# Optimization experiments

Measured on AMD Instinct MI355X. Metric: run time of the kernel, lower is better.

The kernel has to match this reference:

```python
import jax, jax.numpy as jnp
import numpy as np

B, H = 16384, 64          # batch, human_num
SELF_DIM, HUMAN_DIM = 6, 7
D = 32                    # gcn2_w1_dim / embedding dim


def _lin(key, fin, fout):
    return jax.random.normal(key, (fin, fout), jnp.float32) / np.sqrt(fin)


def setup_inputs() -> dict:
    key = jax.random.key(0)
    ks = jax.random.split(key, 40)
    inp = {}
    inp["state"] = jax.random.normal(ks[0], (B, H, SELF_DIM + HUMAN_DIM), jnp.float32)
    inp["dropout"] = 0
    # w_r: mlp(6 -> 64 -> 32, last_relu=True)
    inp["wr_w1"] = _lin(ks[1], SELF_DIM, 64); inp["wr_b1"] = jnp.zeros(64, jnp.float32)
    inp["wr_w2"] = _lin(ks[2], 64, D);        inp["wr_b2"] = jnp.zeros(D, jnp.float32)
    # w_h: mlp(7 -> 64 -> 32, last_relu=True)
    inp["wh_w1"] = _lin(ks[3], HUMAN_DIM, 64); inp["wh_b1"] = jnp.zeros(64, jnp.float32)
    inp["wh_w2"] = _lin(ks[4], 64, D);         inp["wh_b2"] = jnp.zeros(D, jnp.float32)
    # hetero GraphConv weights: per edge type (rh: robot->human, hr: human->robot, hh: human->human),
    # per layer. GraphConv: out = lin_rel(scatter_sum(x_src)) + lin_root(x_dst); lin_root has no bias.
    i = 5
    for L in (1, 2):
        for et in ("rh", "hr", "hh"):
            inp[f"rel_{et}{L}"] = _lin(ks[i], D, D); i += 1
            inp[f"brel_{et}{L}"] = jnp.zeros(D, jnp.float32)
            inp[f"root_{et}{L}"] = _lin(ks[i], D, D); i += 1
    # value_net: mlp(32 -> 150 -> 100 -> 1), no last relu
    inp["vn_w1"] = _lin(ks[i], D, 150);  inp["vn_b1"] = jnp.zeros(150, jnp.float32); i += 1
    inp["vn_w2"] = _lin(ks[i], 150, 100); inp["vn_b2"] = jnp.zeros(100, jnp.float32); i += 1
    inp["vn_w3"] = _lin(ks[i], 100, 1);  inp["vn_b3"] = jnp.zeros(1, jnp.float32)
    return inp


def _hetero_layer(r, h, rel_rh, brel_rh, root_rh, rel_hr, brel_hr, root_hr,
                  rel_hh, brel_hh, root_hh):
    # r: [B, D] robot nodes; h: [B, H, D] human nodes
    sum_h = h.sum(axis=1)  # [B, D]
    # robot receives scatter-sum over all humans (star graph, one robot target)
    new_r = jax.nn.relu(sum_h @ rel_hr + brel_hr + r @ root_hr)
    # each human receives: robot message + sum of all OTHER humans (full graph minus self-loops)
    agg_hh = sum_h[:, None, :] - h  # [B, H, D]
    new_h = jax.nn.relu((r @ rel_rh)[:, None, :] + brel_rh
                        + agg_hh @ rel_hh + brel_hh
                        + h @ root_rh + h @ root_hh)
    return new_r, new_h


def _forward(state, wr_w1, wr_b1, wr_w2, wr_b2, wh_w1, wh_b1, wh_w2, wh_b2,
             rel_rh1, brel_rh1, root_rh1, rel_hr1, brel_hr1, root_hr1,
             rel_hh1, brel_hh1, root_hh1,
             rel_rh2, brel_rh2, root_rh2, rel_hr2, brel_hr2, root_hr2,
             rel_hh2, brel_hh2, root_hh2,
             vn_w1, vn_b1, vn_w2, vn_b2, vn_w3, vn_b3):
    self_state = state[:, 0, :SELF_DIM]        # [B, 6]
    human_states = state[:, :, SELF_DIM:]      # [B, H, 7]
    r = jax.nn.relu(jax.nn.relu(self_state @ wr_w1 + wr_b1) @ wr_w2 + wr_b2)      # [B, D]
    h = jax.nn.relu(jax.nn.relu(human_states @ wh_w1 + wh_b1) @ wh_w2 + wh_b2)    # [B, H, D]
    r, h = _hetero_layer(r, h, rel_rh1, brel_rh1, root_rh1, rel_hr1, brel_hr1,
                         root_hr1, rel_hh1, brel_hh1, root_hh1)
    r, h = _hetero_layer(r, h, rel_rh2, brel_rh2, root_rh2, rel_hr2, brel_hr2,
                         root_hr2, rel_hh2, brel_hh2, root_hh2)
    v = jax.nn.relu(r @ vn_w1 + vn_b1)
    v = jax.nn.relu(v @ vn_w2 + vn_b2)
    return v @ vn_w3 + vn_b3                    # [B, 1]


def reference(state, dropout, wr_w1, wr_b1, wr_w2, wr_b2, wh_w1, wh_b1, wh_w2, wh_b2,
              rel_rh1, brel_rh1, root_rh1, rel_hr1, brel_hr1, root_hr1,
              rel_hh1, brel_hh1, root_hh1,
              rel_rh2, brel_rh2, root_rh2, rel_hr2, brel_hr2, root_hr2,
              rel_hh2, brel_hh2, root_hh2,
              vn_w1, vn_b1, vn_w2, vn_b2, vn_w3, vn_b3):
    # dropout is accepted but unused (matches the torch forward signature)
    return _forward(state, wr_w1, wr_b1, wr_w2, wr_b2, wh_w1, wh_b1, wh_w2, wh_b2,
                    rel_rh1, brel_rh1, root_rh1, rel_hr1, brel_hr1, root_hr1,
                    rel_hh1, brel_hh1, root_hh1,
                    rel_rh2, brel_rh2, root_rh2, rel_hr2, brel_hr2, root_hr2,
                    rel_hh2, brel_hh2, root_hh2,
                    vn_w1, vn_b1, vn_w2, vn_b2, vn_w3, vn_b3)
```

## Files before the change

kernel.cpp:

```cpp
#include <hip/hip_runtime.h>

#define BTOT 16384

typedef __attribute__((ext_vector_type(8))) short bf16x8;
typedef __attribute__((ext_vector_type(4))) float f32x4;

#define MFMA16(a,b,c) __builtin_amdgcn_mfma_f32_16x16x32_bf16((a),(b),(c),0,0,0)

#if __has_builtin(__builtin_amdgcn_cvt_pk_bf16_f32)
typedef __attribute__((ext_vector_type(2))) __bf16 hwbf2;
static __device__ __forceinline__ unsigned pk2(float a, float b) {
    hwbf2 v = __builtin_amdgcn_cvt_pk_bf16_f32(a, b);
    return __builtin_bit_cast(unsigned, v);
}
#else
static __device__ __forceinline__ unsigned pk2(float a, float b) {
    unsigned ua = __float_as_uint(a), ub = __float_as_uint(b);
    unsigned ra = (ua + 0x7FFFu + ((ua >> 16) & 1u)) >> 16;
    unsigned rb = (ub + 0x7FFFu + ((ub >> 16) & 1u)) >> 16;
    return (ra & 0xFFFFu) | (rb << 16);
}
#endif
static __device__ __forceinline__ unsigned short bfhi(float x) {
    return (unsigned short)(pk2(x, 0.f) & 0xFFFFu);
}
static __device__ __forceinline__ float b2f(unsigned short h) {
    return __uint_as_float(((unsigned)h) << 16);
}
static __device__ __forceinline__ short f2s(float x) { return (short)bfhi(x); }
static __device__ __forceinline__ unsigned short bfhi_m(float x) {
    unsigned u = __float_as_uint(x);
    return (unsigned short)((u + 0x7FFFu + ((u >> 16) & 1u)) >> 16);
}
static __device__ __forceinline__ unsigned short bflo_m(float x) {
    unsigned short h = bfhi_m(x);
    return bfhi_m(x - b2f(h));
}
static __device__ __forceinline__ bf16x8 zero8() {
    bf16x8 v;
    #pragma unroll
    for (int i = 0; i < 8; ++i) v[i] = 0;
    return v;
}

__global__ void pack_frags(
    const float* __restrict__ wh_w1, const float* __restrict__ wh_b1,
    const float* __restrict__ wh_w2,
    const float* __restrict__ root_rh1, const float* __restrict__ root_hh1,
    const float* __restrict__ rel_hh1,
    const float* __restrict__ wr_w2,
    const float* __restrict__ rel_hr1, const float* __restrict__ root_hr1,
    const float* __restrict__ rel_rh1,
    const float* __restrict__ rel_hr2, const float* __restrict__ root_hr2,
    const float* __restrict__ vn_w1, const float* __restrict__ vn_w2,
    const float* __restrict__ brel_hr1, const float* __restrict__ brel_rh1,
    const float* __restrict__ brel_hh1, const float* __restrict__ brel_hr2,
    short* __restrict__ pk)
{
    int t = blockIdx.x * blockDim.x + threadIdx.x;
    if (t < 52736) {
        int f = t >> 9, r = t & 511;
        int lane = r >> 3, j = r & 7;
        int q = lane >> 4, c = lane & 15;
        int k = q * 8 + j;
        unsigned short outv;
        if (f < 4) {
            int m = f * 16 + c;
            float v = (k < 7) ? wh_w1[k * 64 + m] : (k == 7 ? wh_b1[m] : 0.f);
            outv = bfhi_m(v);
        } else if (f < 8) {
            int u = f - 4, ks = u >> 1, nt = u & 1;
            int kr = ks * 32 + (j >> 2) * 16 + q * 4 + (j & 3);
            outv = bfhi_m(wh_w2[kr * 32 + nt * 16 + c]);
        } else if (f < 10) {
            int n = (f - 8) * 16 + c;
            int ko = (k >> 1) + ((k & 1) << 4);
            outv = bfhi_m(root_rh1[ko * 32 + n] + root_hh1[ko * 32 + n] - rel_hh1[ko * 32 + n]);
        } else if (f < 22) {
            int u = f - 10, ks = u >> 1, nt = u & 1;
            int kp = ks * 32 + k;
            float w = wr_w2[(kp & 63) * 32 + nt * 16 + c];
            outv = (kp < 128) ? bfhi_m(w) : bflo_m(w);
        } else if (f < 46) {
            int u = f - 22, ks = u >> 2, nt = u & 3;
            int kp = ks * 32 + k, seg = kp >> 5, kk = kp & 31;
            int n2 = (nt & 1) * 16 + c;
            bool sPart = (seg < 2) || (seg == 4);
            const float* W = (nt < 2) ? (sPart ? rel_hr1 : root_hr1)
                                      : (sPart ? rel_hh1 : rel_rh1);
            float w = W[kk * 32 + n2];
            outv = (seg < 4) ? bfhi_m(w) : bflo_m(w);
        } else if (f < 58) {
            int u = f - 46, ks = u >> 1, nt = u & 1;
            int kp = ks * 32 + k, seg = kp >> 5, kk = kp & 31;
            int n = nt * 16 + c;
            bool sPart = (seg < 2) || (seg == 4);
            const float* W = sPart ? rel_hr2 : root_hr2;
            float w = W[kk * 32 + n];
            outv = (seg < 4) ? bfhi_m(w) : bflo_m(w);
        } else if (f < 68) {
            int n = (f - 58) * 16 + c;
            outv = (n < 150) ? bfhi_m(vn_w1[k * 150 + n]) : 0;
        } else {
            int u = f - 68, kt = u / 7, nt = u - kt * 7;
            int kk = kt * 32 + k, n = nt * 16 + c;
            outv = (kk < 150 && n < 100) ? bfhi_m(vn_w2[kk * 100 + n]) : 0;
        }
        pk[t] = (short)outv;
    } else if (t < 52800) {
        int i = t - 52736;
        float* bp = (float*)(pk + 52736);
        bp[i] = (i < 32) ? brel_hr1[i] : brel_rh1[i - 32] + brel_hh1[i - 32];
    } else if (t < 52832) {
        int i = t - 52800;
        float* bp = (float*)(pk + 52864);
        bp[i] = brel_hr2[i];
    }
}

__global__ __launch_bounds__(256) void fused_main(
    const float* __restrict__ state, const short* __restrict__ pk,
    const float* __restrict__ wr_w1, const float* __restrict__ wr_b1,
    const float* __restrict__ wr_b2, const float* __restrict__ wh_b2,
    short* __restrict__ r2buf)
{
    __shared__ __align__(16) short wbuf[4][4096];

    const int tid = threadIdx.x;
    const int wv = tid >> 6, lane = tid & 63;
    const int q = lane >> 4, c = lane & 15;
    const int b = blockIdx.x * 4 + wv;
    const float* st = state + (size_t)b * 832;
    short* T = wbuf[wv];

    const bf16x8* pk16 = (const bf16x8*)pk;
    const float* bg1f = (const float*)(pk + 52736);
    const float* bg2f = (const float*)(pk + 52864);
    const f32x4 z4 = {0.f, 0.f, 0.f, 0.f};

    bf16x8 A1[4], Bh2v[4], Bev[2];
    #pragma unroll
    for (int i = 0; i < 4; ++i) A1[i] = pk16[i * 64 + lane];
    #pragma unroll
    for (int i = 0; i < 4; ++i) Bh2v[i] = pk16[(4 + i) * 64 + lane];
    #pragma unroll
    for (int i = 0; i < 2; ++i) Bev[i] = pk16[(8 + i) * 64 + lane];

    {
        float hf[7];
        #pragma unroll
        for (int m = 0; m < 7; ++m) hf[m] = st[lane * 13 + 6 + m];
        uint4 v = make_uint4(pk2(hf[0], hf[1]), pk2(hf[2], hf[3]),
                             pk2(hf[4], hf[5]), pk2(hf[6], 1.0f));
        *(uint4*)(T + lane * 8) = v;
    }

    float trh;
    {
        float acc = wr_b1[lane];
        #pragma unroll
        for (int m = 0; m < 6; ++m) acc = fmaf(st[m], wr_w1[m * 64 + lane], acc);
        trh = fmaxf(acc, 0.f);
    }

    asm volatile("s_waitcnt lgkmcnt(0)" ::: "memory");

    bf16x8 bx[4];
    #pragma unroll
    for (int ht = 0; ht < 4; ++ht) {
        bf16x8 v = zero8();
        if (q == 0) v = *(const bf16x8*)(T + (ht * 16 + c) * 8);
        bx[ht] = v;
    }

    #pragma unroll
    for (int mhp = 0; mhp < 2; ++mhp) {
        #pragma unroll
        for (int ht = 0; ht < 4; ++ht) {
            f32x4 d0 = MFMA16(A1[2 * mhp + 0], bx[ht], z4);
            f32x4 d1 = MFMA16(A1[2 * mhp + 1], bx[ht], z4);
            d0 = __builtin_elementwise_max(d0, z4);
            d1 = __builtin_elementwise_max(d1, z4);
            uint4 w = make_uint4(pk2(d0[0], d0[1]), pk2(d0[2], d0[3]),
                                 pk2(d1[0], d1[1]), pk2(d1[2], d1[3]));
            int row = ht * 16 + c;
            int p = (mhp * 4 + q) ^ (c & 7);
            *(uint4*)(T + row * 64 + p * 8) = w;
        }
    }

    asm volatile("s_waitcnt lgkmcnt(0)" ::: "memory");

    const float b2a = wh_b2[c], b2b = wh_b2[16 + c];
    const f32x4 b2a4 = {b2a, b2a, b2a, b2a}, b2b4 = {b2b, b2b, b2b, b2b};
    f32x4 psv0 = z4, psv1 = z4;
    #pragma unroll
    for (int mt = 0; mt < 4; ++mt) {
        int row = mt * 16 + c;
        bf16x8 a0 = *(const bf16x8*)(T + row * 64 + ((q ^ (c & 7))) * 8);
        bf16x8 a1 = *(const bf16x8*)(T + row * 64 + (((q + 4) ^ (c & 7))) * 8);
        f32x4 e0 = MFMA16(a0, Bh2v[0], z4); e0 = MFMA16(a1, Bh2v[2], e0);
        f32x4 e1 = MFMA16(a0, Bh2v[1], z4); e1 = MFMA16(a1, Bh2v[3], e1);
        e0 = __builtin_elementwise_max(e0 + b2a4, z4);
        e1 = __builtin_elementwise_max(e1 + b2b4, z4);
        psv0 += e0; psv1 += e1;
        #pragma unroll
        for (int r = 0; r < 4; ++r) {
            int hrow = mt * 16 + q * 4 + r;
            *(unsigned*)(T + hrow * 32 + (((c >> 2) ^ r)) * 8 + (c & 3) * 2) = pk2(e0[r], e1[r]);
        }
    }
    float ps0 = (psv0[0] + psv0[1]) + (psv0[2] + psv0[3]);
    float ps1 = (psv1[0] + psv1[1]) + (psv1[2] + psv1[3]);
    ps0 += __shfl_xor(ps0, 16); ps0 += __shfl_xor(ps0, 32);
    ps1 += __shfl_xor(ps1, 16); ps1 += __shfl_xor(ps1, 32);

    {
        short* SB = T + 3712;
        if (q == 0) {
            unsigned short h0 = bfhi(ps0), h1 = bfhi(ps1);
            SB[c] = (short)h0;        SB[16 + c] = (short)h1;
            SB[32 + c] = (short)bfhi(ps0 - b2f(h0));
            SB[48 + c] = (short)bfhi(ps1 - b2f(h1));
        }
        short* TR = T + 3840;
        unsigned short th = bfhi(trh);
        TR[lane] = (short)th;
        TR[64 + lane] = (short)bfhi(trh - b2f(th));
    }
    __syncthreads();

    const short* rowS = wbuf[c & 3];

    bf16x8 at0 = *(const bf16x8*)(rowS + 3840 + q * 8);
    bf16x8 at1 = *(const bf16x8*)(rowS + 3872 + q * 8);
    bf16x8 at2 = *(const bf16x8*)(rowS + 3904 + q * 8);
    bf16x8 at3 = *(const bf16x8*)(rowS + 3936 + q * 8);
    f32x4 dr0 = z4, dr1 = z4;
    dr0 = MFMA16(at0, pk16[10 * 64 + lane], dr0); dr1 = MFMA16(at0, pk16[11 * 64 + lane], dr1);
    dr0 = MFMA16(at1, pk16[12 * 64 + lane], dr0); dr1 = MFMA16(at1, pk16[13 * 64 + lane], dr1);
    dr0 = MFMA16(at2, pk16[14 * 64 + lane], dr0); dr1 = MFMA16(at2, pk16[15 * 64 + lane], dr1);
    dr0 = MFMA16(at3, pk16[16 * 64 + lane], dr0); dr1 = MFMA16(at3, pk16[17 * 64 + lane], dr1);
    dr0 = MFMA16(at0, pk16[18 * 64 + lane], dr0); dr1 = MFMA16(at0, pk16[19 * 64 + lane], dr1);
    dr0 = MFMA16(at1, pk16[20 * 64 + lane], dr0); dr1 = MFMA16(at1, pk16[21 * 64 + lane], dr1);

    {
        const float wb0 = wr_b2[c], wb1 = wr_b2[16 + c];
        if (q == 0) {
            #pragma unroll
            for (int r = 0; r < 4; ++r) {
                float v0 = fmaxf(dr0[r] + wb0, 0.f), v1 = fmaxf(dr1[r] + wb1, 0.f);
                unsigned short h0 = bfhi(v0), h1 = bfhi(v1);
                T[2048 + r * 32 + c]      = (short)h0;
                T[2048 + r * 32 + 16 + c] = (short)h1;
                T[2176 + r * 32 + c]      = (short)bfhi(v0 - b2f(h0));
                T[2176 + r * 32 + 16 + c] = (short)bfhi(v1 - b2f(h1));
            }
        }
    }
    asm volatile("s_waitcnt lgkmcnt(0)" ::: "memory");

    bf16x8 as0 = *(const bf16x8*)(rowS + 3712 + q * 8);
    bf16x8 as1 = *(const bf16x8*)(rowS + 3744 + q * 8);
    bf16x8 ar0 = *(const bf16x8*)(T + 2048 + (c & 3) * 32 + q * 8);
    bf16x8 ar1 = *(const bf16x8*)(T + 2176 + (c & 3) * 32 + q * 8);
    f32x4 dg[4] = {z4, z4, z4, z4};
    #pragma unroll
    for (int nt = 0; nt < 4; ++nt) dg[nt] = MFMA16(as0, pk16[(22 +  0 + nt) * 64 + lane], dg[nt]);
    #pragma unroll
    for (int nt = 0; nt < 4; ++nt) dg[nt] = MFMA16(as1, pk16[(22 +  4 + nt) * 64 + lane], dg[nt]);
    #pragma unroll
    for (int nt = 0; nt < 4; ++nt) dg[nt] = MFMA16(ar0, pk16[(22 +  8 + nt) * 64 + lane], dg[nt]);
    #pragma unroll
    for (int nt = 0; nt < 4; ++nt) dg[nt] = MFMA16(ar1, pk16[(22 + 12 + nt) * 64 + lane], dg[nt]);
    #pragma unroll
    for (int nt = 0; nt < 4; ++nt) dg[nt] = MFMA16(as0, pk16[(22 + 16 + nt) * 64 + lane], dg[nt]);
    #pragma unroll
    for (int nt = 0; nt < 4; ++nt) dg[nt] = MFMA16(ar0, pk16[(22 + 20 + nt) * 64 + lane], dg[nt]);

    const float c10 = __shfl(dg[2][wv], c) + bg1f[32 + c];
    const float c11 = __shfl(dg[3][wv], c) + bg1f[48 + c];

    {
        if (q == 0) {
            const float gb0 = bg1f[c], gb1 = bg1f[16 + c];
            #pragma unroll
            for (int r = 0; r < 4; ++r) {
                float v0 = fmaxf(dg[0][r] + gb0, 0.f), v1 = fmaxf(dg[1][r] + gb1, 0.f);
                unsigned short h0 = bfhi(v0), h1 = bfhi(v1);
                T[2304 + r * 32 + c]      = (short)h0;
                T[2304 + r * 32 + 16 + c] = (short)h1;
                T[2432 + r * 32 + c]      = (short)bfhi(v0 - b2f(h0));
                T[2432 + r * 32 + 16 + c] = (short)bfhi(v1 - b2f(h1));
            }
        }
    }

    {
        const f32x4 c10v = {c10, c10, c10, c10}, c11v = {c11, c11, c11, c11};
        f32x4 acc0 = z4, acc1 = z4;
        #pragma unroll
        for (int mt = 0; mt < 4; ++mt) {
            int row = mt * 16 + c;
            bf16x8 ah = *(const bf16x8*)(T + row * 32 + ((q ^ (c & 3))) * 8);
            f32x4 g0 = MFMA16(ah, Bev[0], z4);
            f32x4 g1 = MFMA16(ah, Bev[1], z4);
            acc0 += __builtin_elementwise_max(g0 + c10v, z4);
            acc1 += __builtin_elementwise_max(g1 + c11v, z4);
        }
        float t0 = (acc0[0] + acc0[1]) + (acc0[2] + acc0[3]);
        float t1 = (acc1[0] + acc1[1]) + (acc1[2] + acc1[3]);
        t0 += __shfl_xor(t0, 16); t0 += __shfl_xor(t0, 32);
        t1 += __shfl_xor(t1, 16); t1 += __shfl_xor(t1, 32);
        short* G2 = T + 3520;
        if (q == 0) {
            unsigned short h0 = bfhi(t0), h1 = bfhi(t1);
            G2[c] = (short)h0;        G2[16 + c] = (short)h1;
            G2[32 + c] = (short)bfhi(t0 - b2f(h0));
            G2[48 + c] = (short)bfhi(t1 - b2f(h1));
        }
    }
    __syncthreads();

    {
        bf16x8 ag0 = *(const bf16x8*)(rowS + 3520 + q * 8);
        bf16x8 ag1 = *(const bf16x8*)(rowS + 3552 + q * 8);
        bf16x8 agr0 = *(const bf16x8*)(T + 2304 + (c & 3) * 32 + q * 8);
        bf16x8 agr1 = *(const bf16x8*)(T + 2432 + (c & 3) * 32 + q * 8);
        f32x4 d0 = z4, d1 = z4;
        d0 = MFMA16(ag0,  pk16[46 * 64 + lane], d0); d1 = MFMA16(ag0,  pk16[47 * 64 + lane], d1);
        d0 = MFMA16(ag1,  pk16[48 * 64 + lane], d0); d1 = MFMA16(ag1,  pk16[49 * 64 + lane], d1);
        d0 = MFMA16(agr0, pk16[50 * 64 + lane], d0); d1 = MFMA16(agr0, pk16[51 * 64 + lane], d1);
        d0 = MFMA16(agr1, pk16[52 * 64 + lane], d0); d1 = MFMA16(agr1, pk16[53 * 64 + lane], d1);
        d0 = MFMA16(ag0,  pk16[54 * 64 + lane], d0); d1 = MFMA16(ag0,  pk16[55 * 64 + lane], d1);
        d0 = MFMA16(agr0, pk16[56 * 64 + lane], d0); d1 = MFMA16(agr0, pk16[57 * 64 + lane], d1);
        if (q == 0) {
            const float g0 = bg2f[c], g1 = bg2f[16 + c];
            r2buf[b * 32 + c]      = f2s(fmaxf(d0[wv] + g0, 0.f));
            r2buf[b * 32 + 16 + c] = f2s(fmaxf(d1[wv] + g1, 0.f));
        }
    }
}

__global__ __launch_bounds__(256) void head_kernel(
    const short* __restrict__ pk,
    const float* __restrict__ vn_b1, const float* __restrict__ vn_b2,
    const float* __restrict__ vn_w3, const float* __restrict__ vn_b3,
    float* __restrict__ out)
{
    __shared__ __align__(16) short sh_v1[4][16 * 168];
    const int wv = threadIdx.x >> 6, lane = threadIdx.x & 63;
    const int q = lane >> 4, c = lane & 15;
    const int tile = blockIdx.x * 4 + wv;
    const bf16x8* wf = (const bf16x8*)pk;
    const short* r2b = pk + 53248;
    const f32x4 z4 = {0.f, 0.f, 0.f, 0.f};

    bf16x8 a1 = *(const bf16x8*)&r2b[(tile * 16 + c) * 32 + q * 8];
    short* vb = sh_v1[wv];
    #pragma unroll
    for (int nt = 0; nt < 10; ++nt) {
        f32x4 d = MFMA16(a1, wf[(58 + nt) * 64 + lane], z4);
        int n = nt * 16 + c;
        float bias = (n < 150) ? vn_b1[n] : 0.f;
        #pragma unroll
        for (int r = 0; r < 4; ++r) {
            float v = (n < 150) ? fmaxf(d[r] + bias, 0.f) : 0.f;
            vb[(q * 4 + r) * 168 + n] = f2s(v);
        }
    }
    __syncthreads();

    bf16x8 a2[5];
    #pragma unroll
    for (int kt = 0; kt < 5; ++kt)
        a2[kt] = *(const bf16x8*)&vb[c * 168 + kt * 32 + q * 8];

    float racc[4] = {0.f, 0.f, 0.f, 0.f};
    #pragma unroll
    for (int nt = 0; nt < 7; ++nt) {
        f32x4 d = z4;
        #pragma unroll
        for (int kt = 0; kt < 5; ++kt)
            d = MFMA16(a2[kt], wf[(68 + kt * 7 + nt) * 64 + lane], d);
        int n = nt * 16 + c;
        float bias = (n < 100) ? vn_b2[n] : 0.f;
        float w3   = (n < 100) ? vn_w3[n] : 0.f;
        #pragma unroll
        for (int r = 0; r < 4; ++r) racc[r] += fmaxf(d[r] + bias, 0.f) * w3;
    }
    #pragma unroll
    for (int m = 1; m < 16; m <<= 1) {
        #pragma unroll
        for (int r = 0; r < 4; ++r) racc[r] += __shfl_xor(racc[r], m);
    }
    if (c == 0) {
        float b3 = vn_b3[0];
        #pragma unroll
        for (int r = 0; r < 4; ++r) out[tile * 16 + q * 4 + r] = racc[r] + b3;
    }
}

extern "C" void kernel_launch(void* const* d_in, const int* in_sizes, int n_in,
                              void* d_out, int out_size, void* d_ws, size_t ws_size,
                              hipStream_t stream) {
    const float* state    = (const float*)d_in[0];
    const float* wr_w1    = (const float*)d_in[2];
    const float* wr_b1    = (const float*)d_in[3];
    const float* wr_w2    = (const float*)d_in[4];
    const float* wr_b2    = (const float*)d_in[5];
    const float* wh_w1    = (const float*)d_in[6];
    const float* wh_b1    = (const float*)d_in[7];
    const float* wh_w2    = (const float*)d_in[8];
    const float* wh_b2    = (const float*)d_in[9];
    const float* rel_rh1  = (const float*)d_in[10];
    const float* brel_rh1 = (const float*)d_in[11];
    const float* root_rh1 = (const float*)d_in[12];
    const float* rel_hr1  = (const float*)d_in[13];
    const float* brel_hr1 = (const float*)d_in[14];
    const float* root_hr1 = (const float*)d_in[15];
    const float* rel_hh1  = (const float*)d_in[16];
    const float* brel_hh1 = (const float*)d_in[17];
    const float* root_hh1 = (const float*)d_in[18];
    const float* rel_hr2  = (const float*)d_in[22];
    const float* brel_hr2 = (const float*)d_in[23];
    const float* root_hr2 = (const float*)d_in[24];
    const float* vn_w1    = (const float*)d_in[28];
    const float* vn_b1    = (const float*)d_in[29];
    const float* vn_w2    = (const float*)d_in[30];
    const float* vn_b2    = (const float*)d_in[31];
    const float* vn_w3    = (const float*)d_in[32];
    const float* vn_b3    = (const float*)d_in[33];
    float* out = (float*)d_out;
    short* pk  = (short*)d_ws;
    short* r2buf = pk + 53248;

    pack_frags<<<207, 256, 0, stream>>>(wh_w1, wh_b1, wh_w2,
                                        root_rh1, root_hh1, rel_hh1, wr_w2,
                                        rel_hr1, root_hr1, rel_rh1,
                                        rel_hr2, root_hr2, vn_w1, vn_w2,
                                        brel_hr1, brel_rh1, brel_hh1, brel_hr2, pk);
    fused_main<<<BTOT / 4, 256, 0, stream>>>(state, pk, wr_w1, wr_b1, wr_b2, wh_b2, r2buf);
    head_kernel<<<BTOT / 64, 256, 0, stream>>>(pk, vn_b1, vn_b2, vn_w3, vn_b3, out);
}
```

Before: 188.1 us.

## Chain human MLP through registers via transposed MFMA operands, shrink LDS

Recasts the human-embedding MLP and the layer-1 human update as weight-times-activation MFMAs with the weight fragments repacked, so layer-1 outputs stay in registers in operand layout and feed the second matmul directly. This removes the LDS round-trips for the 64-wide hidden and the 32-wide embeddings and cuts per-wave shared memory from 8 KB to about 2.5 KB, which should raise occupancy. In exchange it adds register pressure (16 packed hidden values kept live) and replaces shuffle reductions with a butterfly over four lanes.

```diff
diff --git a/kernel.cpp b/kernel.cpp
--- a/kernel.cpp
+++ b/kernel.cpp
@@ -27,6 +27,7 @@
 static __device__ __forceinline__ float b2f(unsigned short h) {
     return __uint_as_float(((unsigned)h) << 16);
 }
+static __device__ __forceinline__ float lof(float x) { return x - b2f(bfhi(x)); }
 static __device__ __forceinline__ short f2s(float x) { return (short)bfhi(x); }
 static __device__ __forceinline__ unsigned short bfhi_m(float x) {
     unsigned u = __float_as_uint(x);
@@ -41,6 +42,11 @@
     #pragma unroll
     for (int i = 0; i < 8; ++i) v[i] = 0;
     return v;
+}
+static __device__ __forceinline__ bf16x8 mk8(unsigned a, unsigned b, unsigned c, unsigned d) {
+    union { unsigned u[4]; bf16x8 v; } x;
+    x.u[0] = a; x.u[1] = b; x.u[2] = c; x.u[3] = d;
+    return x.v;
 }
 
 __global__ void pack_frags(
@@ -63,19 +69,21 @@
         int lane = r >> 3, j = r & 7;
         int q = lane >> 4, c = lane & 15;
         int k = q * 8 + j;
+        int kap = (j < 4) ? (4 * q + j) : (16 + 4 * q + (j - 4));
         unsigned short outv;
         if (f < 4) {
             int m = f * 16 + c;
             float v = (k < 7) ? wh_w1[k * 64 + m] : (k == 7 ? wh_b1[m] : 0.f);
             outv = bfhi_m(v);
         } else if (f < 8) {
-            int u = f - 4, ks = u >> 1, nt = u & 1;
-            int kr = ks * 32 + (j >> 2) * 16 + q * 4 + (j & 3);
-            outv = bfhi_m(wh_w2[kr * 32 + nt * 16 + c]);
+            int u = f - 4, fo = u >> 1, kf = u & 1;
+            int m = fo * 16 + c;
+            int hid = kf * 32 + kap;
+            outv = bfhi_m(wh_w2[hid * 32 + m]);
         } else if (f < 10) {
-            int n = (f - 8) * 16 + c;
-            int ko = (k >> 1) + ((k & 1) << 4);
-            outv = bfhi_m(root_rh1[ko * 32 + n] + root_hh1[ko * 32 + n] - rel_hh1[ko * 32 + n]);
+            int ot = f - 8;
+            int m = ot * 16 + c;
+            outv = bfhi_m(root_rh1[kap * 32 + m] + root_hh1[kap * 32 + m] - rel_hh1[kap * 32 + m]);
         } else if (f < 22) {
             int u = f - 10, ks = u >> 1, nt = u & 1;
             int kp = ks * 32 + k;
@@ -124,28 +132,21 @@
     const float* __restrict__ wr_b2, const float* __restrict__ wh_b2,
     short* __restrict__ r2buf)
 {
-    __shared__ __align__(16) short wbuf[4][4096];
+    __shared__ __align__(16) short wbuf[4 * 1280];
 
     const int tid = threadIdx.x;
     const int wv = tid >> 6, lane = tid & 63;
     const int q = lane >> 4, c = lane & 15;
     const int b = blockIdx.x * 4 + wv;
     const float* st = state + (size_t)b * 832;
-    short* T = wbuf[wv];
+    short* T = wbuf + wv * 1280;
+    const short* rowS = wbuf + (c & 3) * 1280;
 
     const bf16x8* pk16 = (const bf16x8*)pk;
     const float* bg1f = (const float*)(pk + 52736);
     const float* bg2f = (const float*)(pk + 52864);
     const f32x4 z4 = {0.f, 0.f, 0.f, 0.f};
 
-    bf16x8 A1[4], Bh2v[4], Bev[2];
-    #pragma unroll
-    for (int i = 0; i < 4; ++i) A1[i] = pk16[i * 64 + lane];
-    #pragma unroll
-    for (int i = 0; i < 4; ++i) Bh2v[i] = pk16[(4 + i) * 64 + lane];
-    #pragma unroll
-    for (int i = 0; i < 2; ++i) Bev[i] = pk16[(8 + i) * 64 + lane];
-
     {
         float hf[7];
         #pragma unroll
@@ -155,178 +156,178 @@
         *(uint4*)(T + lane * 8) = v;
     }
 
-    float trh;
     {
         float acc = wr_b1[lane];
         #pragma unroll
         for (int m = 0; m < 6; ++m) acc = fmaf(st[m], wr_w1[m * 64 + lane], acc);
-        trh = fmaxf(acc, 0.f);
+        float trh = fmaxf(acc, 0.f);
+        unsigned short th = bfhi(trh);
+        T[576 + lane] = (short)th;
+        T[640 + lane] = (short)bfhi(trh - b2f(th));
     }
 
     asm volatile("s_waitcnt lgkmcnt(0)" ::: "memory");
 
-    bf16x8 bx[4];
-    #pragma unroll
-    for (int ht = 0; ht < 4; ++ht) {
-        bf16x8 v = zero8();
-        if (q == 0) v = *(const bf16x8*)(T + (ht * 16 + c) * 8);
-        bx[ht] = v;
-    }
-
-    #pragma unroll
-    for (int mhp = 0; mhp < 2; ++mhp) {
-        #pragma unroll
-        for (int ht = 0; ht < 4; ++ht) {
-            f32x4 d0 = MFMA16(A1[2 * mhp + 0], bx[ht], z4);
-            f32x4 d1 = MFMA16(A1[2 * mhp + 1], bx[ht], z4);
-            d0 = __builtin_elementwise_max(d0, z4);
-            d1 = __builtin_elementwise_max(d1, z4);
-            uint4 w = make_uint4(pk2(d0[0], d0[1]), pk2(d0[2], d0[3]),
-                                 pk2(d1[0], d1[1]), pk2(d1[2], d1[3]));
-            int row = ht * 16 + c;
-            int p = (mhp * 4 + q) ^ (c & 7);
-            *(uint4*)(T + row * 64 + p * 8) = w;
-        }
-    }
-
-    asm volatile("s_waitcnt lgkmcnt(0)" ::: "memory");
-
-    const float b2a = wh_b2[c], b2b = wh_b2[16 + c];
-    const f32x4 b2a4 = {b2a, b2a, b2a, b2a}, b2b4 = {b2b, b2b, b2b, b2b};
-    f32x4 psv0 = z4, psv1 = z4;
-    #pragma unroll
-    for (int mt = 0; mt < 4; ++mt) {
-        int row = mt * 16 + c;
-        bf16x8 a0 = *(const bf16x8*)(T + row * 64 + ((q ^ (c & 7))) * 8);
-        bf16x8 a1 = *(const bf16x8*)(T + row * 64 + (((q + 4) ^ (c & 7))) * 8);
-        f32x4 e0 = MFMA16(a0, Bh2v[0], z4); e0 = MFMA16(a1, Bh2v[2], e0);
-        f32x4 e1 = MFMA16(a0, Bh2v[1], z4); e1 = MFMA16(a1, Bh2v[3], e1);
-        e0 = __builtin_elementwise_max(e0 + b2a4, z4);
-        e1 = __builtin_elementwise_max(e1 + b2b4, z4);
-        psv0 += e0; psv1 += e1;
+    bf16x8 A1[4], AW2[4];
+    #pragma unroll
+    for (int i = 0; i < 4; ++i) A1[i] = pk16[i * 64 + lane];
+    #pragma unroll
+    for (int i = 0; i < 4; ++i) AW2[i] = pk16[(4 + i) * 64 + lane];
+    const f32x4 b2v0 = *(const f32x4*)(wh_b2 + 4 * q);
+    const f32x4 b2v1 = *(const f32x4*)(wh_b2 + 16 + 4 * q);
+
+    f32x4 sacc0 = z4, sacc1 = z4;
+    unsigned hP[16];
+    #pragma unroll
+    for (int nt = 0; nt < 4; ++nt) {
+        bf16x8 bx = zero8();
+        if (q == 0) bx = *(const bf16x8*)(T + (nt * 16 + c) * 8);
+        f32x4 d0 = MFMA16(A1[0], bx, z4);
+        f32x4 d1 = MFMA16(A1[1], bx, z4);
+        d0 = __builtin_elementwise_max(d0, z4);
+        d1 = __builtin_elementwise_max(d1, z4);
+        bf16x8 t0 = mk8(pk2(d0[0], d0[1]), pk2(d0[2], d0[3]),
+                        pk2(d1[0], d1[1]), pk2(d1[2], d1[3]));
+        f32x4 e0 = MFMA16(AW2[0], t0, z4);
+        f32x4 e1 = MFMA16(AW2[2], t0, z4);
+        f32x4 d2 = MFMA16(A1[2], bx, z4);
+        f32x4 d3 = MFMA16(A1[3], bx, z4);
+        d2 = __builtin_elementwise_max(d2, z4);
+        d3 = __builtin_elementwise_max(d3, z4);
+        bf16x8 t1 = mk8(pk2(d2[0], d2[1]), pk2(d2[2], d2[3]),
+                        pk2(d3[0], d3[1]), pk2(d3[2], d3[3]));
+        e0 = MFMA16(AW2[1], t1, e0);
+        e1 = MFMA16(AW2[3], t1, e1);
+        e0 = __builtin_elementwise_max(e0 + b2v0, z4);
+        e1 = __builtin_elementwise_max(e1 + b2v1, z4);
+        sacc0 += e0; sacc1 += e1;
+        hP[nt * 4 + 0] = pk2(e0[0], e0[1]); hP[nt * 4 + 1] = pk2(e0[2], e0[3]);
+        hP[nt * 4 + 2] = pk2(e1[0], e1[1]); hP[nt * 4 + 3] = pk2(e1[2], e1[3]);
+    }
+    #pragma unroll
+    for (int mask = 1; mask <= 8; mask <<= 1) {
         #pragma unroll
         for (int r = 0; r < 4; ++r) {
-            int hrow = mt * 16 + q * 4 + r;
-            *(unsigned*)(T + hrow * 32 + (((c >> 2) ^ r)) * 8 + (c & 3) * 2) = pk2(e0[r], e1[r]);
-        }
-    }
-    float ps0 = (psv0[0] + psv0[1]) + (psv0[2] + psv0[3]);
-    float ps1 = (psv1[0] + psv1[1]) + (psv1[2] + psv1[3]);
-    ps0 += __shfl_xor(ps0, 16); ps0 += __shfl_xor(ps0, 32);
-    ps1 += __shfl_xor(ps1, 16); ps1 += __shfl_xor(ps1, 32);
-
-    {
-        short* SB = T + 3712;
-        if (q == 0) {
-            unsigned short h0 = bfhi(ps0), h1 = bfhi(ps1);
-            SB[c] = (short)h0;        SB[16 + c] = (short)h1;
-            SB[32 + c] = (short)bfhi(ps0 - b2f(h0));
-            SB[48 + c] = (short)bfhi(ps1 - b2f(h1));
-        }
-        short* TR = T + 3840;
-        unsigned short th = bfhi(trh);
-        TR[lane] = (short)th;
-        TR[64 + lane] = (short)bfhi(trh - b2f(th));
+            sacc0[r] += __shfl_xor(sacc0[r], mask);
+            sacc1[r] += __shfl_xor(sacc1[r], mask);
+        }
+    }
+    if (c == 0) {
+        *(unsigned*)(T + 512 + 4 * q)          = pk2(sacc0[0], sacc0[1]);
+        *(unsigned*)(T + 512 + 4 * q + 2)      = pk2(sacc0[2], sacc0[3]);
+        *(unsigned*)(T + 512 + 16 + 4 * q)     = pk2(sacc1[0], sacc1[1]);
+        *(unsigned*)(T + 512 + 16 + 4 * q + 2) = pk2(sacc1[2], sacc1[3]);
+        *(unsigned*)(T + 544 + 4 * q)          = pk2(lof(sacc0[0]), lof(sacc0[1]));
+        *(unsigned*)(T + 544 + 4 * q + 2)      = pk2(lof(sacc0[2]), lof(sacc0[3]));
+        *(unsigned*)(T + 544 + 16 + 4 * q)     = pk2(lof(sacc1[0]), lof(sacc1[1]));
+        *(unsigned*)(T + 544 + 16 + 4 * q + 2) = pk2(lof(sacc1[2]), lof(sacc1[3]));
     }
     __syncthreads();
 
-    const short* rowS = wbuf[c & 3];
-
-    bf16x8 at0 = *(const bf16x8*)(rowS + 3840 + q * 8);
-    bf16x8 at1 = *(const bf16x8*)(rowS + 3872 + q * 8);
-    bf16x8 at2 = *(const bf16x8*)(rowS + 3904 + q * 8);
-    bf16x8 at3 = *(const bf16x8*)(rowS + 3936 + q * 8);
-    f32x4 dr0 = z4, dr1 = z4;
-    dr0 = MFMA16(at0, pk16[10 * 64 + lane], dr0); dr1 = MFMA16(at0, pk16[11 * 64 + lane], dr1);
-    dr0 = MFMA16(at1, pk16[12 * 64 + lane], dr0); dr1 = MFMA16(at1, pk16[13 * 64 + lane], dr1);
-    dr0 = MFMA16(at2, pk16[14 * 64 + lane], dr0); dr1 = MFMA16(at2, pk16[15 * 64 + lane], dr1);
-    dr0 = MFMA16(at3, pk16[16 * 64 + lane], dr0); dr1 = MFMA16(at3, pk16[17 * 64 + lane], dr1);
-    dr0 = MFMA16(at0, pk16[18 * 64 + lane], dr0); dr1 = MFMA16(at0, pk16[19 * 64 + lane], dr1);
-    dr0 = MFMA16(at1, pk16[20 * 64 + lane], dr0); dr1 = MFMA16(at1, pk16[21 * 64 + lane], dr1);
-
-    {
+    {
+        bf16x8 at0 = *(const bf16x8*)(rowS + 576 + q * 8);
+        bf16x8 at1 = *(const bf16x8*)(rowS + 608 + q * 8);
+        bf16x8 at2 = *(const bf16x8*)(rowS + 640 + q * 8);
+        bf16x8 at3 = *(const bf16x8*)(rowS + 672 + q * 8);
+        f32x4 dr0 = z4, dr1 = z4;
+        dr0 = MFMA16(at0, pk16[10 * 64 + lane], dr0); dr1 = MFMA16(at0, pk16[11 * 64 + lane], dr1);
+        dr0 = MFMA16(at1, pk16[12 * 64 + lane], dr0); dr1 = MFMA16(at1, pk16[13 * 64 + lane], dr1);
+        dr0 = MFMA16(at2, pk16[14 * 64 + lane], dr0); dr1 = MFMA16(at2, pk16[15 * 64 + lane], dr1);
+        dr0 = MFMA16(at3, pk16[16 * 64 + lane], dr0); dr1 = MFMA16(at3, pk16[17 * 64 + lane], dr1);
+        dr0 = MFMA16(at0, pk16[18 * 64 + lane], dr0); dr1 = MFMA16(at0, pk16[19 * 64 + lane], dr1);
+        dr0 = MFMA16(at1, pk16[20 * 64 + lane], dr0); dr1 = MFMA16(at1, pk16[21 * 64 + lane], dr1);
         const float wb0 = wr_b2[c], wb1 = wr_b2[16 + c];
         if (q == 0) {
             #pragma unroll
             for (int r = 0; r < 4; ++r) {
                 float v0 = fmaxf(dr0[r] + wb0, 0.f), v1 = fmaxf(dr1[r] + wb1, 0.f);
                 unsigned short h0 = bfhi(v0), h1 = bfhi(v1);
-                T[2048 + r * 32 + c]      = (short)h0;
-                T[2048 + r * 32 + 16 + c] = (short)h1;
-                T[2176 + r * 32 + c]      = (short)bfhi(v0 - b2f(h0));
-                T[2176 + r * 32 + 16 + c] = (short)bfhi(v1 - b2f(h1));
+                T[704 + r * 32 + c]      = (short)h0;
+                T[704 + r * 32 + 16 + c] = (short)h1;
+                T[832 + r * 32 + c]      = (short)bfhi(v0 - b2f(h0));
+                T[832 + r * 32 + 16 + c] = (short)bfhi(v1 - b2f(h1));
             }
         }
     }
     asm volatile("s_waitcnt lgkmcnt(0)" ::: "memory");
 
-    bf16x8 as0 = *(const bf16x8*)(rowS + 3712 + q * 8);
-    bf16x8 as1 = *(const bf16x8*)(rowS + 3744 + q * 8);
-    bf16x8 ar0 = *(const bf16x8*)(T + 2048 + (c & 3) * 32 + q * 8);
-    bf16x8 ar1 = *(const bf16x8*)(T + 2176 + (c & 3) * 32 + q * 8);
-    f32x4 dg[4] = {z4, z4, z4, z4};
-    #pragma unroll
-    for (int nt = 0; nt < 4; ++nt) dg[nt] = MFMA16(as0, pk16[(22 +  0 + nt) * 64 + lane], dg[nt]);
-    #pragma unroll
-    for (int nt = 0; nt < 4; ++nt) dg[nt] = MFMA16(as1, pk16[(22 +  4 + nt) * 64 + lane], dg[nt]);
-    #pragma unroll
-    for (int nt = 0; nt < 4; ++nt) dg[nt] = MFMA16(ar0, pk16[(22 +  8 + nt) * 64 + lane], dg[nt]);
-    #pragma unroll
-    for (int nt = 0; nt < 4; ++nt) dg[nt] = MFMA16(ar1, pk16[(22 + 12 + nt) * 64 + lane], dg[nt]);
-    #pragma unroll
-    for (int nt = 0; nt < 4; ++nt) dg[nt] = MFMA16(as0, pk16[(22 + 16 + nt) * 64 + lane], dg[nt]);
-    #pragma unroll
-    for (int nt = 0; nt < 4; ++nt) dg[nt] = MFMA16(ar0, pk16[(22 + 20 + nt) * 64 + lane], dg[nt]);
-
-    const float c10 = __shfl(dg[2][wv], c) + bg1f[32 + c];
-    const float c11 = __shfl(dg[3][wv], c) + bg1f[48 + c];
-
-    {
+    f32x4 c1f0, c1f1;
+    {
+        bf16x8 as0 = *(const bf16x8*)(rowS + 512 + q * 8);
+        bf16x8 as1 = *(const bf16x8*)(rowS + 544 + q * 8);
+        bf16x8 ar0 = *(const bf16x8*)(T + 704 + (c & 3) * 32 + q * 8);
+        bf16x8 ar1 = *(const bf16x8*)(T + 832 + (c & 3) * 32 + q * 8);
+        f32x4 dg[4] = {z4, z4, z4, z4};
+        #pragma unroll
+        for (int nt = 0; nt < 4; ++nt) dg[nt] = MFMA16(as0, pk16[(22 +  0 + nt) * 64 + lane], dg[nt]);
+        #pragma unroll
+        for (int nt = 0; nt < 4; ++nt) dg[nt] = MFMA16(as1, pk16[(22 +  4 + nt) * 64 + lane], dg[nt]);
+        #pragma unroll
+        for (int nt = 0; nt < 4; ++nt) dg[nt] = MFMA16(ar0, pk16[(22 +  8 + nt) * 64 + lane], dg[nt]);
+        #pragma unroll
+        for (int nt = 0; nt < 4; ++nt) dg[nt] = MFMA16(ar1, pk16[(22 + 12 + nt) * 64 + lane], dg[nt]);
+        #pragma unroll
+        for (int nt = 0; nt < 4; ++nt) dg[nt] = MFMA16(as0, pk16[(22 + 16 + nt) * 64 + lane], dg[nt]);
+        #pragma unroll
+        for (int nt = 0; nt < 4; ++nt) dg[nt] = MFMA16(ar0, pk16[(22 + 20 + nt) * 64 + lane], dg[nt]);
+        #pragma unroll
+        for (int r = 0; r < 4; ++r) {
+            c1f0[r] = __shfl(dg[2][wv], 4 * q + r);
+            c1f1[r] = __shfl(dg[3][wv], 4 * q + r);
+        }
+        c1f0 += *(const f32x4*)(bg1f + 32 + 4 * q);
+        c1f1 += *(const f32x4*)(bg1f + 48 + 4 * q);
         if (q == 0) {
             const float gb0 = bg1f[c], gb1 = bg1f[16 + c];
             #pragma unroll
             for (int r = 0; r < 4; ++r) {
                 float v0 = fmaxf(dg[0][r] + gb0, 0.f), v1 = fmaxf(dg[1][r] + gb1, 0.f);
                 unsigned short h0 = bfhi(v0), h1 = bfhi(v1);
-                T[2304 + r * 32 + c]      = (short)h0;
-                T[2304 + r * 32 + 16 + c] = (short)h1;
-                T[2432 + r * 32 + c]      = (short)bfhi(v0 - b2f(h0));
-                T[2432 + r * 32 + 16 + c] = (short)bfhi(v1 - b2f(h1));
+                T[960 + r * 32 + c]       = (short)h0;
+                T[960 + r * 32 + 16 + c]  = (short)h1;
+                T[1088 + r * 32 + c]      = (short)bfhi(v0 - b2f(h0));
+                T[1088 + r * 32 + 16 + c] = (short)bfhi(v1 - b2f(h1));
             }
         }
     }
 
     {
-        const f32x4 c10v = {c10, c10, c10, c10}, c11v = {c11, c11, c11, c11};
-        f32x4 acc0 = z4, acc1 = z4;
-        #pragma unroll
-        for (int mt = 0; mt < 4; ++mt) {
-            int row = mt * 16 + c;
-            bf16x8 ah = *(const bf16x8*)(T + row * 32 + ((q ^ (c & 3))) * 8);
-            f32x4 g0 = MFMA16(ah, Bev[0], z4);
-            f32x4 g1 = MFMA16(ah, Bev[1], z4);
-            acc0 += __builtin_elementwise_max(g0 + c10v, z4);
-            acc1 += __builtin_elementwise_max(g1 + c11v, z4);
-        }
-        float t0 = (acc0[0] + acc0[1]) + (acc0[2] + acc0[3]);
-        float t1 = (acc1[0] + acc1[1]) + (acc1[2] + acc1[3]);
-        t0 += __shfl_xor(t0, 16); t0 += __shfl_xor(t0, 32);
-        t1 += __shfl_xor(t1, 16); t1 += __shfl_xor(t1, 32);
-        short* G2 = T + 3520;
-        if (q == 0) {
-            unsigned short h0 = bfhi(t0), h1 = bfhi(t1);
-            G2[c] = (short)h0;        G2[16 + c] = (short)h1;
-            G2[32 + c] = (short)bfhi(t0 - b2f(h0));
-            G2[48 + c] = (short)bfhi(t1 - b2f(h1));
+        bf16x8 AWe0 = pk16[8 * 64 + lane], AWe1 = pk16[9 * 64 + lane];
+        f32x4 s2a0 = z4, s2a1 = z4;
+        #pragma unroll
+        for (int nt = 0; nt < 4; ++nt) {
+            bf16x8 hb = mk8(hP[nt * 4 + 0], hP[nt * 4 + 1], hP[nt * 4 + 2], hP[nt * 4 + 3]);
+            f32x4 g0 = MFMA16(AWe0, hb, z4);
+            f32x4 g1 = MFMA16(AWe1, hb, z4);
+            s2a0 += __builtin_elementwise_max(g0 + c1f0, z4);
+            s2a1 += __builtin_elementwise_max(g1 + c1f1, z4);
+        }
+        #pragma unroll
+        for (int mask = 1; mask <= 8; mask <<= 1) {
+            #pragma unroll
+            for (int r = 0; r < 4; ++r) {
+                s2a0[r] += __shfl_xor(s2a0[r], mask);
+                s2a1[r] += __shfl_xor(s2a1[r], mask);
+            }
+        }
+        if (c == 0) {
+            *(unsigned*)(T + 1216 + 4 * q)          = pk2(s2a0[0], s2a0[1]);
+            *(unsigned*)(T + 1216 + 4 * q + 2)      = pk2(s2a0[2], s2a0[3]);
+            *(unsigned*)(T + 1216 + 16 + 4 * q)     = pk2(s2a1[0], s2a1[1]);
+            *(unsigned*)(T + 1216 + 16 + 4 * q + 2) = pk2(s2a1[2], s2a1[3]);
+            *(unsigned*)(T + 1248 + 4 * q)          = pk2(lof(s2a0[0]), lof(s2a0[1]));
+            *(unsigned*)(T + 1248 + 4 * q + 2)      = pk2(lof(s2a0[2]), lof(s2a0[3]));
+            *(unsigned*)(T + 1248 + 16 + 4 * q)     = pk2(lof(s2a1[0]), lof(s2a1[1]));
+            *(unsigned*)(T + 1248 + 16 + 4 * q + 2) = pk2(lof(s2a1[2]), lof(s2a1[3]));
         }
     }
     __syncthreads();
 
     {
-        bf16x8 ag0 = *(const bf16x8*)(rowS + 3520 + q * 8);
-        bf16x8 ag1 = *(const bf16x8*)(rowS + 3552 + q * 8);
-        bf16x8 agr0 = *(const bf16x8*)(T + 2304 + (c & 3) * 32 + q * 8);
-        bf16x8 agr1 = *(const bf16x8*)(T + 2432 + (c & 3) * 32 + q * 8);
+        bf16x8 ag0  = *(const bf16x8*)(rowS + 1216 + q * 8);
+        bf16x8 ag1  = *(const bf16x8*)(rowS + 1248 + q * 8);
+        bf16x8 agr0 = *(const bf16x8*)(T + 960 + (c & 3) * 32 + q * 8);
+        bf16x8 agr1 = *(const bf16x8*)(T + 1088 + (c & 3) * 32 + q * 8);
         f32x4 d0 = z4, d1 = z4;
         d0 = MFMA16(ag0,  pk16[46 * 64 + lane], d0); d1 = MFMA16(ag0,  pk16[47 * 64 + lane], d1);
         d0 = MFMA16(ag1,  pk16[48 * 64 + lane], d0); d1 = MFMA16(ag1,  pk16[49 * 64 + lane], d1);
```

Result: slower. 200.4 us (+6.5%).
